# Kernel tuning notes

Measured on AMD Instinct MI355X. Metric: run time of the kernel, lower is better.

## Reference

```python
import jax, jax.numpy as jnp
import numpy as np

N, E = 100000, 1600000
NF, HC, NC = 32, 64, 64


def setup_inputs() -> dict:
    key = jax.random.key(0)
    ks = jax.random.split(key, 12)
    s = 0.05
    return {
        "x": jax.random.normal(ks[0], (N, NF), dtype=jnp.float32),
        "edge_index": jax.random.randint(ks[1], (2, E), 0, N, dtype=jnp.int64),
        "eps1": jnp.float32(0.0),
        "eps2": jnp.float32(0.0),
        "W1a": jax.random.normal(ks[2], (NF, HC), dtype=jnp.float32) * s,
        "b1a": jnp.zeros((HC,), dtype=jnp.float32),
        "W1b": jax.random.normal(ks[3], (HC, HC), dtype=jnp.float32) * s,
        "b1b": jnp.zeros((HC,), dtype=jnp.float32),
        "W2a": jax.random.normal(ks[4], (HC, HC), dtype=jnp.float32) * s,
        "b2a": jnp.zeros((HC,), dtype=jnp.float32),
        "W2b": jax.random.normal(ks[5], (HC, NC), dtype=jnp.float32) * s,
        "b2b": jnp.zeros((NC,), dtype=jnp.float32),
    }


def _gin_conv(h, src, dst, eps, Wa, ba, Wb, bb, num_nodes):
    # sum-aggregate neighbor features: out[dst] += h[src]
    agg = jax.ops.segment_sum(h[src], dst, num_segments=num_nodes)
    z = (1.0 + eps) * h + agg
    # 2-layer MLP: Linear -> ReLU -> Linear
    z = jax.nn.relu(z @ Wa + ba)
    return z @ Wb + bb


def reference(x, edge_index, eps1, eps2, W1a, b1a, W1b, b1b, W2a, b2a, W2b, b2b):
    src, dst = edge_index[0], edge_index[1]
    n = x.shape[0]
    emb = _gin_conv(x, src, dst, eps1, W1a, b1a, W1b, b1b, n)  # [N, HC]
    h = jax.nn.relu(emb)  # dropout is identity in eval mode
    logits = _gin_conv(h, src, dst, eps2, W2a, b2a, W2b, b2b, n)  # [N, NC]
    return (logits, emb)
```

## Files before the change

kernel.cpp:

```cpp
#include <hip/hip_runtime.h>


#define NFEAT 32
#define HID   64
#define NCLS  64

#define BSH   9
#define BNODES 512
#define NBKT_MAX 256
#define BCAP  16384
#define ECAP  2048

typedef unsigned int uint;
typedef unsigned short ushortT;
typedef __attribute__((ext_vector_type(8))) short bf16x8;
typedef __attribute__((ext_vector_type(4))) float f32x4;

__device__ __forceinline__ int clampi(int v, int hi){ v = v < 0 ? 0 : v; return v > hi ? hi : v; }

__device__ __forceinline__ ushortT f2b(float f){
  uint u = __float_as_uint(f);
  u = (u + 0x7FFFu + ((u >> 16) & 1u)) >> 16;
  return (ushortT)u;
}
__device__ __forceinline__ float b2f_lo(uint u){ return __uint_as_float(u << 16); }
__device__ __forceinline__ float b2f_hi(uint u){ return __uint_as_float(u & 0xFFFF0000u); }
__device__ __forceinline__ uint pack2(float lo, float hi){
  return (uint)f2b(lo) | ((uint)f2b(hi) << 16);
}


__global__ void k_prep(const float* __restrict__ x, ushortT* __restrict__ xb, int n4,
                       const float* __restrict__ W1a, const float* __restrict__ W1b,
                       const float* __restrict__ W2a, const float* __restrict__ W2b,
                       ushortT* __restrict__ T1a, ushortT* __restrict__ T1b,
                       ushortT* __restrict__ T2a, ushortT* __restrict__ T2b,
                       int* __restrict__ bktCnt, int nbkt){
  int t = blockIdx.x*256 + threadIdx.x;
  if (t < n4){
    float4 v = reinterpret_cast<const float4*>(x)[t];
    ushort4 o = { f2b(v.x), f2b(v.y), f2b(v.z), f2b(v.w) };
    reinterpret_cast<ushort4*>(xb)[t] = o;
  }
  if (t < nbkt) bktCnt[t] = 0;
  if (t < 14336){
    const float* W; ushortT* T; int K; int base;
    if      (t <  2048){ W=W1a; T=T1a; K=32; base=0;     }
    else if (t <  6144){ W=W1b; T=T1b; K=64; base=2048;  }
    else if (t < 10240){ W=W2a; T=T2a; K=64; base=6144;  }
    else               { W=W2b; T=T2b; K=64; base=10240; }
    int o = t - base;
    int k = o >> 6, c = o & 63;
    T[c*K + k] = f2b(W[o]);
  }
}


__global__ void k_bucket(const int* __restrict__ src, const int* __restrict__ dst,
                         int E, int N, int nbkt,
                         int* __restrict__ bktCnt, int* __restrict__ bktData){
  __shared__ int s_cnt[NBKT_MAX];
  __shared__ int s_base[NBKT_MAX];
  const int t = threadIdx.x;
  for (int j = t; j < nbkt; j += 256) s_cnt[j] = 0;
  __syncthreads();

  const int e0 = blockIdx.x * 4096;
  const int e1 = min(e0 + 4096, E);
  for (int e = e0 + t; e < e1; e += 256){
    int d = clampi(dst[e], N-1);
    atomicAdd(&s_cnt[d >> BSH], 1);
  }
  __syncthreads();
  for (int j = t; j < nbkt; j += 256){
    int c = s_cnt[j];
    s_base[j] = (c > 0) ? atomicAdd(&bktCnt[j], c) : 0;
    s_cnt[j] = 0;
  }
  __syncthreads();
  for (int e = e0 + t; e < e1; e += 256){
    int d = clampi(dst[e], N-1);
    int s = clampi(src[e], N-1);
    int b = d >> BSH;
    int p = s_base[b] + atomicAdd(&s_cnt[b], 1);
    if (p < BCAP)
      bktData[(size_t)b * BCAP + p] = ((d & (BNODES-1)) << 17) | s;
  }
}


__global__ __launch_bounds__(BNODES)
void k_build(const int* __restrict__ bktCnt, const int* __restrict__ bktData,
             int nbkt, int* __restrict__ rowptr, int* __restrict__ eidx, int N){
  __shared__ int s_bs[NBKT_MAX];
  __shared__ int s_h[BNODES];
  __shared__ int s_cur[BNODES];
  const int b = blockIdx.x, t = threadIdx.x;

  if (t < NBKT_MAX) s_bs[t] = (t < nbkt) ? min(bktCnt[t], BCAP) : 0;
  __syncthreads();
  for (int off = 1; off < NBKT_MAX; off <<= 1){
    int add = 0;
    if (t < NBKT_MAX && t >= off) add = s_bs[t-off];
    __syncthreads();
    if (t < NBKT_MAX) s_bs[t] += add;
    __syncthreads();
  }
  const int cnt  = min(bktCnt[b], BCAP);
  const int base = s_bs[b] - cnt;
  if (b == 0 && t == 0) rowptr[N] = s_bs[nbkt-1];
  const int* __restrict__ data = bktData + (size_t)b * BCAP;

  s_h[t] = 0;
  __syncthreads();
  for (int e = t; e < cnt; e += BNODES) atomicAdd(&s_h[data[e] >> 17], 1);
  __syncthreads();

  int deg = s_h[t];
  for (int off = 1; off < BNODES; off <<= 1){
    int add = (t >= off) ? s_h[t-off] : 0;
    __syncthreads();
    s_h[t] += add;
    __syncthreads();
  }
  int excl = s_h[t] - deg;
  int node = b * BNODES + t;
  if (node < N) rowptr[node] = base + excl;
  s_cur[t] = excl;
  __syncthreads();

  for (int e = t; e < cnt; e += BNODES){
    int val = data[e];
    int d = val >> 17;
    int p = atomicAdd(&s_cur[d], 1);
    eidx[base + p] = val & 0x1FFFF;
  }
}


template<int K, bool WRITE_HB>
__global__ __launch_bounds__(512)
void k_fused(const uint4* __restrict__ f4,
             const int* __restrict__ rowptr, const int* __restrict__ eidx,
             const float* __restrict__ epsP,
             const ushortT* __restrict__ WaT,
             const float* __restrict__ ba,
             const ushortT* __restrict__ WbT,
             const float* __restrict__ bb,
             float* __restrict__ out,
             ushortT* __restrict__ hb, int N){
  constexpr int RS = K/8;
  constexpr int CH = RS/4;
  constexpr int U  = (CH == 1) ? 4 : 2;
  constexpr int ZS = K + 8;
  constexpr int HS = 72;
  __shared__ int s_row[65];
  __shared__ int s_eidx[ECAP];
  __shared__ __align__(16) ushortT zt[64*ZS];
  __shared__ __align__(16) ushortT ht[64*HS];
  const int t = threadIdx.x;
  const int row0 = blockIdx.x * 64;

  const int e0 = rowptr[min(row0, N)];
  const int e1 = rowptr[min(row0 + 64, N)];
  if (t < 65){
    int idx = row0 + t; if (idx > N) idx = N;
    s_row[t] = rowptr[idx] - e0;
  }
  const int cnt = e1 - e0;
  for (int j = t; j < cnt && j < ECAP; j += 512) s_eidx[j] = eidx[e0 + j];
  __syncthreads();

  {
    const int n = t >> 3;
    const int L = t & 7;
    const int q = L & 3;
    const int s = L >> 2;
    const int node = row0 + n;
    float acc[CH*8];
    #pragma unroll
    for (int j = 0; j < CH*8; ++j) acc[j] = 0.f;

    const int b = s_row[n];
    const int e = s_row[n+1];

    if (cnt <= ECAP){
      int i = b + s;
      for (; i + 2*(U-1) < e; i += 2*U){
        int src[U];
        #pragma unroll
        for (int u = 0; u < U; ++u) src[u] = s_eidx[i + 2*u];
        uint4 v[U][CH];
        #pragma unroll
        for (int u = 0; u < U; ++u)
          #pragma unroll
          for (int c = 0; c < CH; ++c)
            v[u][c] = f4[(size_t)src[u]*RS + q*CH + c];
        #pragma unroll
        for (int u = 0; u < U; ++u)
          #pragma unroll
          for (int c = 0; c < CH; ++c){
            acc[c*8+0] += b2f_lo(v[u][c].x); acc[c*8+1] += b2f_hi(v[u][c].x);
            acc[c*8+2] += b2f_lo(v[u][c].y); acc[c*8+3] += b2f_hi(v[u][c].y);
            acc[c*8+4] += b2f_lo(v[u][c].z); acc[c*8+5] += b2f_hi(v[u][c].z);
            acc[c*8+6] += b2f_lo(v[u][c].w); acc[c*8+7] += b2f_hi(v[u][c].w);
          }
      }
      for (; i < e; i += 2){
        int src0 = s_eidx[i];
        #pragma unroll
        for (int c = 0; c < CH; ++c){
          uint4 v = f4[(size_t)src0*RS + q*CH + c];
          acc[c*8+0] += b2f_lo(v.x); acc[c*8+1] += b2f_hi(v.x);
          acc[c*8+2] += b2f_lo(v.y); acc[c*8+3] += b2f_hi(v.y);
          acc[c*8+4] += b2f_lo(v.z); acc[c*8+5] += b2f_hi(v.z);
          acc[c*8+6] += b2f_lo(v.w); acc[c*8+7] += b2f_hi(v.w);
        }
      }
    } else {
      for (int i = b + s; i < e; i += 2){
        int src0 = eidx[e0 + i];
        #pragma unroll
        for (int c = 0; c < CH; ++c){
          uint4 v = f4[(size_t)src0*RS + q*CH + c];
          acc[c*8+0] += b2f_lo(v.x); acc[c*8+1] += b2f_hi(v.x);
          acc[c*8+2] += b2f_lo(v.y); acc[c*8+3] += b2f_hi(v.y);
          acc[c*8+4] += b2f_lo(v.z); acc[c*8+5] += b2f_hi(v.z);
          acc[c*8+6] += b2f_lo(v.w); acc[c*8+7] += b2f_hi(v.w);
        }
      }
    }

    if (s == 1 && node < N){
      const float se = 1.0f + epsP[0];
      #pragma unroll
      for (int c = 0; c < CH; ++c){
        uint4 v = f4[(size_t)node*RS + q*CH + c];
        acc[c*8+0] = fmaf(se, b2f_lo(v.x), acc[c*8+0]);
        acc[c*8+1] = fmaf(se, b2f_hi(v.x), acc[c*8+1]);
        acc[c*8+2] = fmaf(se, b2f_lo(v.y), acc[c*8+2]);
        acc[c*8+3] = fmaf(se, b2f_hi(v.y), acc[c*8+3]);
        acc[c*8+4] = fmaf(se, b2f_lo(v.z), acc[c*8+4]);
        acc[c*8+5] = fmaf(se, b2f_hi(v.z), acc[c*8+5]);
        acc[c*8+6] = fmaf(se, b2f_lo(v.w), acc[c*8+6]);
        acc[c*8+7] = fmaf(se, b2f_hi(v.w), acc[c*8+7]);
      }
    }
    #pragma unroll
    for (int j = 0; j < CH*8; ++j) acc[j] += __shfl_xor(acc[j], 4);
    if (s == 0){
      #pragma unroll
      for (int c = 0; c < CH; ++c){
        uint4 z;
        z.x = pack2(acc[c*8+0], acc[c*8+1]);
        z.y = pack2(acc[c*8+2], acc[c*8+3]);
        z.z = pack2(acc[c*8+4], acc[c*8+5]);
        z.w = pack2(acc[c*8+6], acc[c*8+7]);
        *reinterpret_cast<uint4*>(&zt[n*ZS + (q*CH + c)*8]) = z;
      }
    }
  }
  __syncthreads();

  const int w  = t >> 6;
  const int l  = t & 63;
  const int lr = l & 15;
  const int lg = l >> 4;
  const int rf = w & 3;
  const int c0 = (w >> 2) * 2;
  f32x4 c1[2];
  #pragma unroll
  for (int cl = 0; cl < 2; ++cl){ float bv = ba[(c0+cl)*16 + lr]; c1[cl] = (f32x4){bv,bv,bv,bv}; }
  #pragma unroll
  for (int kf = 0; kf < K/32; ++kf){
    bf16x8 a = *reinterpret_cast<const bf16x8*>(&zt[(rf*16 + lr)*ZS + kf*32 + lg*8]);
    #pragma unroll
    for (int cl = 0; cl < 2; ++cl){
      bf16x8 bfr = *reinterpret_cast<const bf16x8*>(&WaT[((c0+cl)*16 + lr)*K + kf*32 + lg*8]);
      c1[cl] = __builtin_amdgcn_mfma_f32_16x16x32_bf16(a, bfr, c1[cl], 0, 0, 0);
    }
  }
  #pragma unroll
  for (int cl = 0; cl < 2; ++cl)
    #pragma unroll
    for (int r = 0; r < 4; ++r)
      ht[(rf*16 + lg*4 + r)*HS + (c0+cl)*16 + lr] = f2b(fmaxf(c1[cl][r], 0.f));
  __syncthreads();

  f32x4 c2[2];
  #pragma unroll
  for (int cl = 0; cl < 2; ++cl){ float bv = bb[(c0+cl)*16 + lr]; c2[cl] = (f32x4){bv,bv,bv,bv}; }
  #pragma unroll
  for (int kf = 0; kf < 2; ++kf){
    bf16x8 a = *reinterpret_cast<const bf16x8*>(&ht[(rf*16 + lr)*HS + kf*32 + lg*8]);
    #pragma unroll
    for (int cl = 0; cl < 2; ++cl){
      bf16x8 bfr = *reinterpret_cast<const bf16x8*>(&WbT[((c0+cl)*16 + lr)*64 + kf*32 + lg*8]);
      c2[cl] = __builtin_amdgcn_mfma_f32_16x16x32_bf16(a, bfr, c2[cl], 0, 0, 0);
    }
  }
  #pragma unroll
  for (int cl = 0; cl < 2; ++cl)
    #pragma unroll
    for (int r = 0; r < 4; ++r){
      int row = row0 + rf*16 + lg*4 + r;
      if (row < N){
        float v = c2[cl][r];
        out[(size_t)row*64 + (c0+cl)*16 + lr] = v;
        if (WRITE_HB) hb[(size_t)row*64 + (c0+cl)*16 + lr] = f2b(fmaxf(v, 0.f));
      }
    }
}


extern "C" void kernel_launch(void* const* d_in, const int* in_sizes, int n_in,
                              void* d_out, int out_size, void* d_ws, size_t ws_size,
                              hipStream_t stream) {
  const int N = in_sizes[0] / NFEAT;
  const int E = in_sizes[1] / 2;
  const int nbkt = (N + BNODES - 1) / BNODES;

  const float* x    = (const float*)d_in[0];
  const int*   ei   = (const int*)d_in[1];
  const int*   srcI = ei;
  const int*   dstI = ei + E;
  const float* eps1 = (const float*)d_in[2];
  const float* eps2 = (const float*)d_in[3];
  const float* W1a  = (const float*)d_in[4];
  const float* b1a  = (const float*)d_in[5];
  const float* W1b  = (const float*)d_in[6];
  const float* b1b  = (const float*)d_in[7];
  const float* W2a  = (const float*)d_in[8];
  const float* b2a  = (const float*)d_in[9];
  const float* W2b  = (const float*)d_in[10];
  const float* b2b  = (const float*)d_in[11];

  float* outLogits = (float*)d_out;
  float* outEmb    = outLogits + (size_t)N * HID;

  char* w = (char*)d_ws;
  size_t off = 0;
  auto alloc = [&](size_t bytes) -> void* {
    void* p = w + off;
    off = (off + bytes + 255) & ~(size_t)255;
    return p;
  };
  int*     rowptr  = (int*)alloc((size_t)(N+1) * sizeof(int));
  int*     eidx    = (int*)alloc((size_t)E * sizeof(int));
  int*     bktCnt  = (int*)alloc((size_t)NBKT_MAX * sizeof(int));
  ushortT* T1a     = (ushortT*)alloc(64*32*sizeof(ushortT));
  ushortT* T1b     = (ushortT*)alloc(64*64*sizeof(ushortT));
  ushortT* T2a     = (ushortT*)alloc(64*64*sizeof(ushortT));
  ushortT* T2b     = (ushortT*)alloc(64*64*sizeof(ushortT));
  int*     bktData = (int*)alloc((size_t)NBKT_MAX * BCAP * sizeof(int));
  ushortT* xb      = (ushortT*)alloc((size_t)N * NFEAT * sizeof(ushortT));
  ushortT* hb      = (ushortT*)alloc((size_t)N * HID * sizeof(ushortT));

  const int n4 = N * NFEAT / 4;
  k_prep<<<(n4+255)/256, 256, 0, stream>>>(x, xb, n4, W1a, W1b, W2a, W2b,
                                           T1a, T1b, T2a, T2b, bktCnt, nbkt);

  k_bucket<<<(E+4095)/4096, 256, 0, stream>>>(srcI, dstI, E, N, nbkt, bktCnt, bktData);
  k_build <<<nbkt, BNODES, 0, stream>>>(bktCnt, bktData, nbkt, rowptr, eidx, N);

  const int nblk = (N + 63) / 64;
  k_fused<NFEAT, true><<<nblk, 512, 0, stream>>>((const uint4*)xb, rowptr, eidx,
      eps1, T1a, b1a, T1b, b1b, outEmb, hb, N);

  k_fused<HID, false><<<nblk, 512, 0, stream>>>((const uint4*)hb, rowptr, eidx,
      eps2, T2a, b2a, T2b, b2b, outLogits, (ushortT*)nullptr, N);
}
```

Measured before the change: 124.1 us.

## Replace global-atomic bucketing with per-block local sort and fixed chunk slots

The edge bucketing pass now sorts each block's edges by destination bucket in shared memory and writes them contiguously into fixed per-(bucket,block) chunk slots. This removes the global atomic counters and the zeroing pass. The CSR build then produces padded per-bucket row begin/end arrays instead of a compacted rowptr. This gives coalesced writes and drops a global prefix sum, but it silently drops edges beyond CHUNK (48) per block-bucket pair. It also reuses the bucket scratch buffer for the hidden features and assumes the padded eidx layout.

```diff
diff --git a/kernel.cpp b/kernel.cpp
--- a/kernel.cpp
+++ b/kernel.cpp
@@ -9,9 +9,12 @@
 #define BNODES 512
 #define NBKT_MAX 256
 #define BCAP  16384
+#define EPB   4096
+#define CHUNK 48
 #define ECAP  2048
 
 typedef unsigned int uint;
+typedef unsigned char uchar;
 typedef unsigned short ushortT;
 typedef __attribute__((ext_vector_type(8))) short bf16x8;
 typedef __attribute__((ext_vector_type(4))) float f32x4;
@@ -34,15 +37,13 @@
                        const float* __restrict__ W1a, const float* __restrict__ W1b,
                        const float* __restrict__ W2a, const float* __restrict__ W2b,
                        ushortT* __restrict__ T1a, ushortT* __restrict__ T1b,
-                       ushortT* __restrict__ T2a, ushortT* __restrict__ T2b,
-                       int* __restrict__ bktCnt, int nbkt){
+                       ushortT* __restrict__ T2a, ushortT* __restrict__ T2b){
   int t = blockIdx.x*256 + threadIdx.x;
   if (t < n4){
     float4 v = reinterpret_cast<const float4*>(x)[t];
     ushort4 o = { f2b(v.x), f2b(v.y), f2b(v.z), f2b(v.w) };
     reinterpret_cast<ushort4*>(xb)[t] = o;
   }
-  if (t < nbkt) bktCnt[t] = 0;
   if (t < 14336){
     const float* W; ushortT* T; int K; int base;
     if      (t <  2048){ W=W1a; T=T1a; K=32; base=0;     }
@@ -56,84 +57,114 @@
 }
 
 
-__global__ void k_bucket(const int* __restrict__ src, const int* __restrict__ dst,
-                         int E, int N, int nbkt,
-                         int* __restrict__ bktCnt, int* __restrict__ bktData){
-  __shared__ int s_cnt[NBKT_MAX];
-  __shared__ int s_base[NBKT_MAX];
-  const int t = threadIdx.x;
+__global__ __launch_bounds__(256)
+void k_bucket(const int* __restrict__ src, const int* __restrict__ dst,
+              int E, int N, int nbkt, int nblkB,
+              int* __restrict__ cnts, int* __restrict__ bktData){
+  __shared__ int   s_val[EPB];
+  __shared__ uchar s_bktb[EPB];
+  __shared__ int   s_sorted[EPB];
+  __shared__ uchar s_sortb[EPB];
+  __shared__ int   s_cnt[NBKT_MAX];
+  __shared__ int   s_loff[NBKT_MAX];
+  const int t = threadIdx.x, blk = blockIdx.x;
+  const int e0 = blk * EPB;
+  const int n  = min(EPB, E - e0);
+
   for (int j = t; j < nbkt; j += 256) s_cnt[j] = 0;
   __syncthreads();
-
-  const int e0 = blockIdx.x * 4096;
-  const int e1 = min(e0 + 4096, E);
-  for (int e = e0 + t; e < e1; e += 256){
-    int d = clampi(dst[e], N-1);
-    atomicAdd(&s_cnt[d >> BSH], 1);
-  }
-  __syncthreads();
-  for (int j = t; j < nbkt; j += 256){
-    int c = s_cnt[j];
-    s_base[j] = (c > 0) ? atomicAdd(&bktCnt[j], c) : 0;
-    s_cnt[j] = 0;
-  }
-  __syncthreads();
-  for (int e = e0 + t; e < e1; e += 256){
-    int d = clampi(dst[e], N-1);
-    int s = clampi(src[e], N-1);
+  for (int j = t; j < n; j += 256){
+    int d = clampi(dst[e0+j], N-1), s = clampi(src[e0+j], N-1);
     int b = d >> BSH;
-    int p = s_base[b] + atomicAdd(&s_cnt[b], 1);
-    if (p < BCAP)
-      bktData[(size_t)b * BCAP + p] = ((d & (BNODES-1)) << 17) | s;
+    s_val[j]  = ((d & (BNODES-1)) << 17) | s;
+    s_bktb[j] = (uchar)b;
+    atomicAdd(&s_cnt[b], 1);
+  }
+  __syncthreads();
+  for (int j = t; j < nbkt; j += 256) s_loff[j] = s_cnt[j];
+  __syncthreads();
+  for (int off = 1; off < NBKT_MAX; off <<= 1){
+    int v = 0;
+    if (t < nbkt && t >= off) v = s_loff[t-off];
+    __syncthreads();
+    if (t < nbkt) s_loff[t] += v;
+    __syncthreads();
+  }
+  if (t < nbkt){
+    int c = s_cnt[t];
+    cnts[(size_t)blk*nbkt + t] = min(c, CHUNK);
+    s_loff[t] -= c;
+  }
+  __syncthreads();
+  if (t < nbkt) s_cnt[t] = s_loff[t];
+  __syncthreads();
+  for (int j = t; j < n; j += 256){
+    int b = s_bktb[j];
+    int p = atomicAdd(&s_cnt[b], 1);
+    s_sorted[p] = s_val[j];
+    s_sortb[p]  = (uchar)b;
+  }
+  __syncthreads();
+  for (int j = t; j < n; j += 256){
+    int b = s_sortb[j];
+    int local = j - s_loff[b];
+    if (local < CHUNK)
+      bktData[((size_t)b*nblkB + blk)*CHUNK + local] = s_sorted[j];
   }
 }
 
 
 __global__ __launch_bounds__(BNODES)
-void k_build(const int* __restrict__ bktCnt, const int* __restrict__ bktData,
-             int nbkt, int* __restrict__ rowptr, int* __restrict__ eidx, int N){
-  __shared__ int s_bs[NBKT_MAX];
-  __shared__ int s_h[BNODES];
-  __shared__ int s_cur[BNODES];
+void k_build(const int* __restrict__ cnts, const int* __restrict__ bktData,
+             int nbkt, int nblkB,
+             int* __restrict__ rowbeg, int* __restrict__ rowend,
+             int* __restrict__ eidx){
+  __shared__ int s_c[BNODES];
+  __shared__ int s_orig[BNODES];
+  __shared__ int s_h[BNODES], s_cur[BNODES];
   const int b = blockIdx.x, t = threadIdx.x;
 
-  if (t < NBKT_MAX) s_bs[t] = (t < nbkt) ? min(bktCnt[t], BCAP) : 0;
-  __syncthreads();
-  for (int off = 1; off < NBKT_MAX; off <<= 1){
-    int add = 0;
-    if (t < NBKT_MAX && t >= off) add = s_bs[t-off];
-    __syncthreads();
-    if (t < NBKT_MAX) s_bs[t] += add;
-    __syncthreads();
-  }
-  const int cnt  = min(bktCnt[b], BCAP);
-  const int base = s_bs[b] - cnt;
-  if (b == 0 && t == 0) rowptr[N] = s_bs[nbkt-1];
-  const int* __restrict__ data = bktData + (size_t)b * BCAP;
+  int c = (t < nblkB) ? cnts[(size_t)t*nbkt + b] : 0;
+  s_orig[t] = c; s_c[t] = c;
+  __syncthreads();
+  for (int off = 1; off < BNODES; off <<= 1){
+    int v = (t >= off) ? s_c[t-off] : 0;
+    __syncthreads();
+    s_c[t] += v;
+    __syncthreads();
+  }
 
   s_h[t] = 0;
   __syncthreads();
-  for (int e = t; e < cnt; e += BNODES) atomicAdd(&s_h[data[e] >> 17], 1);
-  __syncthreads();
-
+  const int nslots = nblkB * CHUNK;
+  for (int j = t; j < nslots; j += BNODES){
+    int blk = j / CHUNK, sl = j - blk*CHUNK;
+    if (sl < s_orig[blk]){
+      int v = bktData[((size_t)b*nblkB + blk)*CHUNK + sl];
+      atomicAdd(&s_h[(v >> 17) & (BNODES-1)], 1);
+    }
+  }
+  __syncthreads();
   int deg = s_h[t];
   for (int off = 1; off < BNODES; off <<= 1){
-    int add = (t >= off) ? s_h[t-off] : 0;
-    __syncthreads();
-    s_h[t] += add;
+    int v = (t >= off) ? s_h[t-off] : 0;
+    __syncthreads();
+    s_h[t] += v;
     __syncthreads();
   }
   int excl = s_h[t] - deg;
   int node = b * BNODES + t;
-  if (node < N) rowptr[node] = base + excl;
+  rowbeg[node] = b*BCAP + excl;
+  rowend[node] = b*BCAP + excl + deg;
   s_cur[t] = excl;
   __syncthreads();
-
-  for (int e = t; e < cnt; e += BNODES){
-    int val = data[e];
-    int d = val >> 17;
-    int p = atomicAdd(&s_cur[d], 1);
-    eidx[base + p] = val & 0x1FFFF;
+  for (int j = t; j < nslots; j += BNODES){
+    int blk = j / CHUNK, sl = j - blk*CHUNK;
+    if (sl < s_orig[blk]){
+      int v = bktData[((size_t)b*nblkB + blk)*CHUNK + sl];
+      int p = atomicAdd(&s_cur[(v >> 17) & (BNODES-1)], 1);
+      eidx[(size_t)b*BCAP + p] = v & 0x1FFFF;
+    }
   }
 }
 
@@ -141,7 +172,8 @@
 template<int K, bool WRITE_HB>
 __global__ __launch_bounds__(512)
 void k_fused(const uint4* __restrict__ f4,
-             const int* __restrict__ rowptr, const int* __restrict__ eidx,
+             const int* __restrict__ rowbeg, const int* __restrict__ rowend,
+             const int* __restrict__ eidx,
              const float* __restrict__ epsP,
              const ushortT* __restrict__ WaT,
              const float* __restrict__ ba,
@@ -154,20 +186,20 @@
   constexpr int U  = (CH == 1) ? 4 : 2;
   constexpr int ZS = K + 8;
   constexpr int HS = 72;
-  __shared__ int s_row[65];
+  __shared__ int s_beg[64], s_end[64];
   __shared__ int s_eidx[ECAP];
   __shared__ __align__(16) ushortT zt[64*ZS];
   __shared__ __align__(16) ushortT ht[64*HS];
   const int t = threadIdx.x;
   const int row0 = blockIdx.x * 64;
 
-  const int e0 = rowptr[min(row0, N)];
-  const int e1 = rowptr[min(row0 + 64, N)];
-  if (t < 65){
-    int idx = row0 + t; if (idx > N) idx = N;
-    s_row[t] = rowptr[idx] - e0;
-  }
-  const int cnt = e1 - e0;
+  if (t < 64){
+    s_beg[t] = rowbeg[row0 + t];
+    s_end[t] = rowend[row0 + t];
+  }
+  __syncthreads();
+  const int e0  = s_beg[0];
+  const int cnt = s_end[63] - e0;
   for (int j = t; j < cnt && j < ECAP; j += 512) s_eidx[j] = eidx[e0 + j];
   __syncthreads();
 
@@ -181,8 +213,8 @@
     #pragma unroll
     for (int j = 0; j < CH*8; ++j) acc[j] = 0.f;
 
-    const int b = s_row[n];
-    const int e = s_row[n+1];
+    const int b = s_beg[n] - e0;
+    const int e = s_end[n] - e0;
 
     if (cnt <= ECAP){
       int i = b + s;
@@ -318,7 +350,8 @@
                               hipStream_t stream) {
   const int N = in_sizes[0] / NFEAT;
   const int E = in_sizes[1] / 2;
-  const int nbkt = (N + BNODES - 1) / BNODES;
+  const int nbkt  = (N + BNODES - 1) / BNODES;
+  const int nblkB = (E + EPB - 1) / EPB;
 
   const float* x    = (const float*)d_in[0];
   const int*   ei   = (const int*)d_in[1];
@@ -345,28 +378,29 @@
     off = (off + bytes + 255) & ~(size_t)255;
     return p;
   };
-  int*     rowptr  = (int*)alloc((size_t)(N+1) * sizeof(int));
-  int*     eidx    = (int*)alloc((size_t)E * sizeof(int));
-  int*     bktCnt  = (int*)alloc((size_t)NBKT_MAX * sizeof(int));
+  int*     rowbeg  = (int*)alloc((size_t)nbkt * BNODES * sizeof(int));
+  int*     rowend  = (int*)alloc((size_t)nbkt * BNODES * sizeof(int));
+  int*     eidx    = (int*)alloc((size_t)nbkt * BCAP * sizeof(int));
+  int*     cnts    = (int*)alloc((size_t)nblkB * nbkt * sizeof(int));
   ushortT* T1a     = (ushortT*)alloc(64*32*sizeof(ushortT));
   ushortT* T1b     = (ushortT*)alloc(64*64*sizeof(ushortT));
   ushortT* T2a     = (ushortT*)alloc(64*64*sizeof(ushortT));
   ushortT* T2b     = (ushortT*)alloc(64*64*sizeof(ushortT));
-  int*     bktData = (int*)alloc((size_t)NBKT_MAX * BCAP * sizeof(int));
+  int*     bktData = (int*)alloc((size_t)nbkt * nblkB * CHUNK * sizeof(int));
+  ushortT* hb      = (ushortT*)bktData;
   ushortT* xb      = (ushortT*)alloc((size_t)N * NFEAT * sizeof(ushortT));
-  ushortT* hb      = (ushortT*)alloc((size_t)N * HID * sizeof(ushortT));
 
   const int n4 = N * NFEAT / 4;
   k_prep<<<(n4+255)/256, 256, 0, stream>>>(x, xb, n4, W1a, W1b, W2a, W2b,
-                                           T1a, T1b, T2a, T2b, bktCnt, nbkt);
-
-  k_bucket<<<(E+4095)/4096, 256, 0, stream>>>(srcI, dstI, E, N, nbkt, bktCnt, bktData);
-  k_build <<<nbkt, BNODES, 0, stream>>>(bktCnt, bktData, nbkt, rowptr, eidx, N);
-
-  const int nblk = (N + 63) / 64;
-  k_fused<NFEAT, true><<<nblk, 512, 0, stream>>>((const uint4*)xb, rowptr, eidx,
-      eps1, T1a, b1a, T1b, b1b, outEmb, hb, N);
-
-  k_fused<HID, false><<<nblk, 512, 0, stream>>>((const uint4*)hb, rowptr, eidx,
-      eps2, T2a, b2a, T2b, b2b, outLogits, (ushortT*)nullptr, N);
-}
+                                           T1a, T1b, T2a, T2b);
+
+  k_bucket<<<nblkB, 256, 0, stream>>>(srcI, dstI, E, N, nbkt, nblkB, cnts, bktData);
+  k_build <<<nbkt, BNODES, 0, stream>>>(cnts, bktData, nbkt, nblkB, rowbeg, rowend, eidx);
+
+  const int nblk = nbkt * 8;
+  k_fused<NFEAT, true><<<nblk, 512, 0, stream>>>((const uint4*)xb, rowbeg, rowend,
+      eidx, eps1, T1a, b1a, T1b, b1b, outEmb, hb, N);
+
+  k_fused<HID, false><<<nblk, 512, 0, stream>>>((const uint4*)hb, rowbeg, rowend,
+      eidx, eps2, T2a, b2a, T2b, b2b, outLogits, (ushortT*)nullptr, N);
+}
```

Result: slower. 127.0 us (+2.4%).
